# Kernel optimization log

Hardware: AMD Instinct MI355X
Metric: run time of the kernel (lower is better)

The kernel has to match this reference:

```python
import jax, jax.numpy as jnp
import numpy as np

B = 4096          # agents
T = 16            # input_length
GH, GW = 13, 13   # grid_size
ENC = 64          # encoder_size
INP = 32          # input_embedding
DYN = 32          # dynamic_embedding
SOC = 64          # soc_embedding_size
DEC = 128         # decoder_size
K = 32            # occupied grid cells (neighbors) per agent
NNB = B * K       # total neighbors


def lrelu(x):
    return jnp.where(x >= 0, x, 0.1 * x)


def lstm_scan(x, Wih, Whh, bih, bhh, return_seq=False):
    # PyTorch LSTM gate order: i, f, g, o. x: [T, N, in]
    N = x.shape[1]
    H = Whh.shape[1]
    xg = jnp.einsum('tni,gi->tng', x, Wih) + bih + bhh  # precompute input part

    def step(carry, g_in):
        h, c = carry
        g = g_in + h @ Whh.T
        i, f, gg, o = jnp.split(g, 4, axis=-1)
        c = jax.nn.sigmoid(f) * c + jax.nn.sigmoid(i) * jnp.tanh(gg)
        h = jax.nn.sigmoid(o) * jnp.tanh(c)
        return (h, c), (h if return_seq else None)

    h0 = jnp.zeros((N, H), x.dtype)
    (h, _), hs = jax.lax.scan(step, (h0, h0), xg)
    return hs if return_seq else h


def setup_inputs() -> dict:
    key = jax.random.key(0)
    ks = jax.random.split(key, 16)

    def lin(k, o, i):
        k1, k2 = jax.random.split(k)
        s = 1.0 / np.sqrt(i)
        return (jax.random.uniform(k1, (o, i), minval=-s, maxval=s),
                jax.random.uniform(k2, (o,), minval=-s, maxval=s))

    W_inp, b_inp = lin(ks[0], INP, 2)
    W_dym, b_dym = lin(ks[1], DYN, ENC)
    W_sp, b_sp = lin(ks[2], SOC, GH * GW * ENC)
    W_out, b_out = lin(ks[3], 5, DEC)
    Wih, bih = lin(ks[4], 4 * ENC, INP)
    Whh, bhh = lin(ks[5], 4 * ENC, ENC)
    dWih, dbih = lin(ks[6], 4 * DEC, SOC + DYN)
    dWhh, dbhh = lin(ks[7], 4 * DEC, DEC)

    hist_batch = jax.random.normal(ks[8], (T, B, 2), dtype=jnp.float32)
    nbrs_batch = jax.random.normal(ks[9], (T, NNB, 2), dtype=jnp.float32)

    # mask: exactly K occupied grid cells per agent; each occupied cell is True
    # across all ENC channels so masked_scatter_ places exactly one neighbor
    # hidden vector per occupied cell (True count == NNB * ENC).
    rng = np.random.default_rng(0)
    idx = np.argsort(rng.random((B, GH * GW)), axis=1)[:, :K]
    cells = np.zeros((B, GH * GW), dtype=bool)
    np.put_along_axis(cells, idx, True, axis=1)
    mask_batch = jnp.asarray(
        np.broadcast_to(cells.reshape(B, GH, GW, 1), (B, GH, GW, ENC)))

    return dict(hist_batch=hist_batch, nbrs_batch=nbrs_batch,
                W_inp=W_inp, b_inp=b_inp, Wih=Wih, Whh=Whh, bih=bih, bhh=bhh,
                W_dym=W_dym, b_dym=b_dym, W_sp=W_sp, b_sp=b_sp,
                dWih=dWih, dWhh=dWhh, dbih=dbih, dbhh=dbhh,
                W_out=W_out, b_out=b_out, mask_batch=mask_batch)


def reference(hist_batch, nbrs_batch, W_inp, b_inp, Wih, Whh, bih, bhh,
              W_dym, b_dym, W_sp, b_sp, dWih, dWhh, dbih, dbhh,
              W_out, b_out, mask_batch):
    # history encoder
    hist_h = lstm_scan(lrelu(hist_batch @ W_inp.T + b_inp), Wih, Whh, bih, bhh)  # [B,ENC]
    hist_enc = lrelu(hist_h @ W_dym.T + b_dym)                                   # [B,DYN]

    # neighbor encoder (shared LSTM)
    nbrs_h = lstm_scan(lrelu(nbrs_batch @ W_inp.T + b_inp), Wih, Whh, bih, bhh)  # [NNB,ENC]

    # masked_scatter_: fill True positions (row-major order) with nbrs_h values
    mflat = mask_batch.reshape(-1)
    src = nbrs_h.reshape(-1)
    pos = jnp.cumsum(mflat) - 1
    soc = jnp.where(mflat, src[jnp.clip(pos, 0, src.shape[0] - 1)],
                    jnp.zeros((), src.dtype))
    soc = soc.reshape(mask_batch.shape)                 # [B,GH,GW,ENC]
    soc = soc.transpose(0, 3, 2, 1)                     # permute(0,3,2,1)
    soc = soc.reshape(soc.shape[0], -1)                 # [B, ENC*GW*GH]
    social = lrelu(soc @ W_sp.T + b_sp)                 # [B,SOC]

    enc = jnp.concatenate([hist_enc, social], axis=1)   # [B, DYN+SOC]
    enc_seq = jnp.broadcast_to(enc, (T,) + enc.shape)   # repeat(T,1,1)
    dec = lstm_scan(enc_seq, dWih, dWhh, dbih, dbhh, return_seq=True)  # [T,B,DEC]
    out = dec.transpose(1, 0, 2) @ W_out.T + b_out      # [B,T,5]

    # outputActivation: mu_x, mu_y, exp(sig_x), exp(sig_y), tanh(rho)
    muX, muY, sX, sY, rho = jnp.split(out, 5, axis=2)
    return jnp.concatenate(
        [muX, muY, jnp.exp(sX), jnp.exp(sY), jnp.tanh(rho)], axis=2)
```

## Files before the change

kernel.cpp:

```cpp
#include <hip/hip_runtime.h>
#include <hip/hip_bf16.h>

typedef _Float16 half8 __attribute__((ext_vector_type(8)));
typedef _Float16 half2v __attribute__((ext_vector_type(2)));
typedef float f32x4 __attribute__((ext_vector_type(4)));

constexpr float L2E   = 1.44269504088896340736f;
constexpr float SC_LO = 4096.0f;
constexpr float IV_LO = 1.0f / 4096.0f;

#define MFMA16(a,b,c) __builtin_amdgcn_mfma_f32_16x16x32_f16((a),(b),(c),0,0,0)

__device__ __forceinline__ float fexp2(float x){ float r; asm("v_exp_f32 %0, %1":"=v"(r):"v"(x)); return r; }
__device__ __forceinline__ float frcp(float x){ float r; asm("v_rcp_f32 %0, %1":"=v"(r):"v"(x)); return r; }

__device__ __forceinline__ float sigm_s(float y){ return frcp(1.0f + fexp2(-y)); }
__device__ __forceinline__ float tanh_s(float y){ return 1.0f - 2.0f*frcp(fexp2(y) + 1.0f); }

__global__ __launch_bounds__(256, 2)
void mega_enc_kernel(const float* __restrict__ xh,
                     const float* __restrict__ xn,
                     const float* __restrict__ W_inp,
                     const float* __restrict__ b_inp,
                     const float* __restrict__ Wih,
                     const float* __restrict__ Whh,
                     const float* __restrict__ bih,
                     const float* __restrict__ bhh,
                     const float* __restrict__ W_sp,
                     const void*  __restrict__ mask_raw,
                     float* __restrict__ outh,
                     float* __restrict__ outn,
                     _Float16* __restrict__ WspT,
                     unsigned char* __restrict__ pos)
{
    __shared__ _Float16 h_hi[2][64*72];
    __shared__ _Float16 h_ls[2][64*72];
    const int tid = threadIdx.x;
    const int bid = blockIdx.x;

    if (bid >= 2112) {
        if (bid < 2112 + 2704) {
            const int idx = (bid - 2112) * 256 + tid;
            if (idx < 64 * 10816) {
                const int s = idx / 10816, cidx = idx % 10816;
                const int e = cidx / 169, p = cidx % 169;
                WspT[((size_t)p*64 + e)*64 + s] = (_Float16)W_sp[idx];
            }
        } else {
            const int agent = (bid - 4816) * 4 + (tid >> 6);
            const int l = tid & 63;
            if (agent < 4096) {
                if (l < 32) pos[agent*32 + l] = 0;
                const unsigned char* raw = (const unsigned char*)mask_raw;
                const int* mi = (const int*)mask_raw;
                int mism = 0;
#pragma unroll
                for (int ch = 0; ch < 3; ++ch) {
                    const int cc = ch*64 + l;
                    if (cc < 169) {
                        const unsigned char b0 = raw[cc*64], b1 = raw[cc*64 + 1];
                        mism |= (b0 != 0 && b1 == 0) ? 1 : 0;
                    }
                }
                const bool is_i32 = (__ballot(mism != 0) != 0ull);
                int base = 0;
#pragma unroll
                for (int ch = 0; ch < 3; ++ch) {
                    const int cc = ch*64 + l;
                    bool occ = false;
                    if (cc < 169) {
                        const size_t ei = (size_t)agent * 10816 + (size_t)cc * 64;
                        occ = is_i32 ? (mi[ei] != 0) : (raw[ei] != 0);
                    }
                    const unsigned long long bal = __ballot(occ);
                    if (occ) {
                        const int rank = base + __popcll(bal & ((1ull << l) - 1ull));
                        const int gh = cc / 13, gw = cc % 13;
                        if (rank < 32)
                            pos[agent*32 + rank] = (unsigned char)(gw*13 + gh);
                    }
                    base += __popcll(bal);
                }
            }
        }
        return;
    }

    const int w   = tid >> 6;
    const int l   = tid & 63;
    const int l15 = l & 15, lhi = l >> 4;

    const bool is_hist = (bid < 64);
    const float* x = is_hist ? xh : xn;
    float* out     = is_hist ? outh : outn;
    const int N    = is_hist ? 4096 : 131072;
    const int rbase = (is_hist ? bid : (bid - 64)) * 64;

    half8 whhH[4][2], whhLs[4][2];
    half8 wihH[4];
    float bias[4];
#pragma unroll
    for (int g = 0; g < 4; ++g) {
        const int col = 16*(w + 4*g) + l15;
        const float sc = (g == 2) ? 2.0f*L2E : L2E;
#pragma unroll
        for (int kh = 0; kh < 2; ++kh)
#pragma unroll
            for (int j = 0; j < 8; ++j) {
                const float v = Whh[col*64 + kh*32 + lhi*8 + j] * sc;
                const _Float16 hi = (_Float16)v;
                whhH[g][kh][j]  = hi;
                whhLs[g][kh][j] = (_Float16)((v - (float)hi) * SC_LO);
            }
#pragma unroll
        for (int j = 0; j < 8; ++j)
            wihH[g][j] = (_Float16)(Wih[col*32 + lhi*8 + j] * sc);
        bias[g] = (bih[col] + bhh[col]) * sc;
    }
    half2v w01[8];
    float bb[8];
#pragma unroll
    for (int j = 0; j < 8; ++j) {
        const int k = lhi*8 + j;
        w01[j][0] = (_Float16)W_inp[k*2 + 0];
        w01[j][1] = (_Float16)W_inp[k*2 + 1];
        bb[j] = b_inp[k];
    }

    float c[4][4];
#pragma unroll
    for (int m = 0; m < 4; ++m)
#pragma unroll
        for (int j = 0; j < 4; ++j) c[m][j] = 0.0f;

    const float2* xp = (const float2*)x;
    float2 xc[4];
#pragma unroll
    for (int m = 0; m < 4; ++m)
        xc[m] = xp[(size_t)0*N + rbase + 16*m + l15];

#pragma unroll 1
    for (int t = 0; t < 16; ++t) {
        const int rdb = (t + 1) & 1;
        const int wrb = t & 1;
#pragma unroll
        for (int m = 0; m < 4; ++m) {
            half8 eh;
#pragma unroll
            for (int j = 0; j < 8; ++j) {
                float v = xc[m].x * (float)w01[j][0] + xc[m].y * (float)w01[j][1] + bb[j];
                v = fmaxf(v, 0.1f * v);
                eh[j] = (_Float16)v;
            }
            f32x4 a0[4], a2[4];
#pragma unroll
            for (int g = 0; g < 4; ++g) {
                a0[g] = (f32x4){bias[g], bias[g], bias[g], bias[g]};
                a2[g] = (f32x4){0.f, 0.f, 0.f, 0.f};
            }
#pragma unroll
            for (int g = 0; g < 4; ++g)
                a0[g] = MFMA16(eh, wihH[g], a0[g]);
            if (t > 0) {
#pragma unroll
                for (int kh = 0; kh < 2; ++kh) {
                    const int off = (16*m + l15)*72 + kh*32 + lhi*8;
                    half8 ah = *(const half8*)&h_hi[rdb][off];
                    half8 as = *(const half8*)&h_ls[rdb][off];
#pragma unroll
                    for (int g = 0; g < 4; ++g) {
                        a0[g] = MFMA16(ah, whhH[g][kh],  a0[g]);
                        a2[g] = MFMA16(ah, whhLs[g][kh], a2[g]);
                        a2[g] = MFMA16(as, whhH[g][kh],  a2[g]);
                    }
                }
            }
#pragma unroll
            for (int j = 0; j < 4; ++j) {
                const float pi = a0[0][j] + a2[0][j]*IV_LO;
                const float pf = a0[1][j] + a2[1][j]*IV_LO;
                const float pg = a0[2][j] + a2[2][j]*IV_LO;
                const float po = a0[3][j] + a2[3][j]*IV_LO;
                const float si = sigm_s(pi);
                const float sf = sigm_s(pf);
                const float tg = tanh_s(pg);
                const float so = sigm_s(po);
                const float cc = sf * c[m][j] + si * tg;
                c[m][j] = cc;
                const float hv = so * tanh_s(2.0f*L2E*cc);
                const int idx = (16*m + lhi*4 + j)*72 + 16*w + l15;
                const _Float16 hi = (_Float16)hv;
                h_hi[wrb][idx] = hi;
                h_ls[wrb][idx] = (_Float16)((hv - (float)hi) * SC_LO);
            }
        }
        __syncthreads();
        if (t < 15) {
#pragma unroll
            for (int m = 0; m < 4; ++m)
                xc[m] = xp[(size_t)(t+1)*N + rbase + 16*m + l15];
        }
    }
    {
        const int row = tid >> 2, c0 = (tid & 3) * 16;
        const size_t g = (size_t)(rbase + row) * 64 + c0;
#pragma unroll
        for (int i = 0; i < 16; ++i) {
            const int idx = row*72 + c0 + i;
            out[g + i] = (float)h_hi[1][idx] + (float)h_ls[1][idx] * IV_LO;
        }
    }
}

__global__ __launch_bounds__(256)
void social_kernel(const float* __restrict__ nh,
                   const float* __restrict__ hh,
                   const _Float16* __restrict__ WspT,
                   const float* __restrict__ b_sp,
                   const float* __restrict__ W_dym,
                   const float* __restrict__ b_dym,
                   const unsigned char* __restrict__ pos,
                   float* __restrict__ enc)
{
    __shared__ float part[4][64];
    __shared__ unsigned char pl[32];
    const int tid = threadIdx.x, b = blockIdx.x;
    if (tid < 32) {
        const int p = pos[b*32 + tid];
        pl[tid] = (unsigned char)(p > 168 ? 0 : p);
    }
    __syncthreads();
    const int s = tid & 63, kq = tid >> 6;
    float a = 0.f;
    for (int kk = 0; kk < 8; ++kk) {
        const int k = kq*8 + kk;
        const float* nr = nh + ((size_t)b*32 + k) * 64;
        const _Float16* wp = WspT + (size_t)pl[k] * 4096 + s;
#pragma unroll
        for (int e = 0; e < 64; ++e) a += nr[e] * (float)wp[(size_t)e * 64];
    }
    part[kq][s] = a;
    __syncthreads();
    if (tid < 64) {
        const float v = part[0][tid] + part[1][tid] + part[2][tid] + part[3][tid] + b_sp[tid];
        enc[(size_t)b * 96 + 32 + tid] = fmaxf(v, 0.1f * v);
    } else if (tid >= 64 && tid < 96) {
        const int so = tid - 64;
        float ah = b_dym[so];
        const float* hr = hh + (size_t)b * 64;
        const float* wr = W_dym + (size_t)so * 64;
#pragma unroll
        for (int e = 0; e < 64; ++e) ah += hr[e] * wr[e];
        enc[(size_t)b * 96 + so] = fmaxf(ah, 0.1f * ah);
    }
}

__global__ __launch_bounds__(512, 1)
void decoder_kernel(const float* __restrict__ enc,
                    const float* __restrict__ dWih,
                    const float* __restrict__ dWhh,
                    const float* __restrict__ dbih,
                    const float* __restrict__ dbhh,
                    const float* __restrict__ W_out,
                    const float* __restrict__ b_out,
                    float* __restrict__ outp)
{
    __shared__ float enc_lds[16*100];
    __shared__ _Float16 hh_t[16*136];
    __shared__ _Float16 hl_t[16*136];
    __shared__ float wout[5*132];
    __shared__ float bout[5];
    __shared__ float part[16][5][4];
    const int tid = threadIdx.x;
    const int w = tid >> 6, l = tid & 63, l15 = l & 15, lhi = l >> 4;
    const int rb = blockIdx.x * 16;

    if (tid < 384) {
        const int row = tid / 24, ch = tid % 24;
        *(float4*)&enc_lds[row*100 + ch*4] = *(const float4*)&enc[(size_t)(rb + row)*96 + ch*4];
    }
    for (int i = tid; i < 640; i += 512) { const int j = i / 128, e = i % 128; wout[j*132 + e] = W_out[i]; }
    if (tid < 5) bout[tid] = b_out[tid];
    __syncthreads();

    half8 whhH[4][4], whhLs[4][4];
    f32x4 xg0[4], xg2[4];
#pragma unroll
    for (int g = 0; g < 4; ++g) {
        const int col = 16*(8*g + w) + l15;
        const float sc = (g == 2) ? 2.0f*L2E : L2E;
#pragma unroll
        for (int kh = 0; kh < 4; ++kh)
#pragma unroll
            for (int j = 0; j < 8; ++j) {
                const float v = dWhh[col*128 + kh*32 + lhi*8 + j] * sc;
                const _Float16 hi = (_Float16)v;
                whhH[g][kh][j]  = hi;
                whhLs[g][kh][j] = (_Float16)((v - (float)hi) * SC_LO);
            }
        const float bv = (dbih[col] + dbhh[col]) * sc;
        xg0[g] = (f32x4){bv, bv, bv, bv};
        xg2[g] = (f32x4){0.f, 0.f, 0.f, 0.f};
    }
#pragma unroll
    for (int kh = 0; kh < 3; ++kh) {
        half8 eh, els;
#pragma unroll
        for (int j = 0; j < 8; ++j) {
            const float v = enc_lds[l15*100 + kh*32 + lhi*8 + j];
            const _Float16 hi = (_Float16)v;
            eh[j]  = hi;
            els[j] = (_Float16)((v - (float)hi) * SC_LO);
        }
#pragma unroll
        for (int g = 0; g < 4; ++g) {
            const int col = 16*(8*g + w) + l15;
            const float sc = (g == 2) ? 2.0f*L2E : L2E;
            half8 bH, bLs;
#pragma unroll
            for (int j = 0; j < 8; ++j) {
                const float v = dWih[col*96 + kh*32 + lhi*8 + j] * sc;
                const _Float16 hi = (_Float16)v;
                bH[j]  = hi;
                bLs[j] = (_Float16)((v - (float)hi) * SC_LO);
            }
            xg0[g] = MFMA16(eh,  bH,  xg0[g]);
            xg2[g] = MFMA16(eh,  bLs, xg2[g]);
            xg2[g] = MFMA16(els, bH,  xg2[g]);
        }
    }
    f32x4 xg[4];
#pragma unroll
    for (int g = 0; g < 4; ++g)
#pragma unroll
        for (int j = 0; j < 4; ++j) xg[g][j] = xg0[g][j] + xg2[g][j]*IV_LO;

    float c[4] = {0.f, 0.f, 0.f, 0.f};
#pragma unroll 1
    for (int t = 0; t < 16; ++t) {
        f32x4 a0[4], a2[4];
#pragma unroll
        for (int g = 0; g < 4; ++g) { a0[g] = xg[g]; a2[g] = (f32x4){0.f,0.f,0.f,0.f}; }
        if (t > 0) {
#pragma unroll
            for (int kh = 0; kh < 4; ++kh) {
                const int off = l15*136 + kh*32 + lhi*8;
                half8 ah = *(const half8*)&hh_t[off];
                half8 as = *(const half8*)&hl_t[off];
#pragma unroll
                for (int g = 0; g < 4; ++g) {
                    a0[g] = MFMA16(ah, whhH[g][kh],  a0[g]);
                    a2[g] = MFMA16(ah, whhLs[g][kh], a2[g]);
                    a2[g] = MFMA16(as, whhH[g][kh],  a2[g]);
                }
            }
        }
        float hnew[4];
#pragma unroll
        for (int j = 0; j < 4; ++j) {
            const float pi = a0[0][j] + a2[0][j]*IV_LO;
            const float pf = a0[1][j] + a2[1][j]*IV_LO;
            const float pg = a0[2][j] + a2[2][j]*IV_LO;
            const float po = a0[3][j] + a2[3][j]*IV_LO;
            const float si = sigm_s(pi);
            const float sf = sigm_s(pf);
            const float tg = tanh_s(pg);
            const float so = sigm_s(po);
            const float cc = sf * c[j] + si * tg;
            c[j] = cc;
            hnew[j] = so * tanh_s(2.0f*L2E*cc);
        }
        __syncthreads();
#pragma unroll
        for (int j = 0; j < 4; ++j) {
            const int idx = (lhi*4 + j)*136 + 16*w + l15;
            const float v = hnew[j];
            const _Float16 hi = (_Float16)v;
            hh_t[idx] = hi;
            hl_t[idx] = (_Float16)((v - (float)hi) * SC_LO);
        }
        __syncthreads();
        if (tid < 320) {
            const int row = tid / 20, rem = tid % 20, j5 = rem / 4, q = rem % 4;
            float pacc = 0.0f;
#pragma unroll
            for (int e = 0; e < 32; ++e) {
                const int idx = row*136 + q*32 + e;
                pacc += ((float)hh_t[idx] + (float)hl_t[idx]*IV_LO) * wout[j5*132 + q*32 + e];
            }
            part[row][j5][q] = pacc;
        }
        __syncthreads();
        if (tid < 80) {
            const int row = tid / 5, j5 = tid % 5;
            float v = part[row][j5][0] + part[row][j5][1] + part[row][j5][2] + part[row][j5][3] + bout[j5];
            if (j5 == 2 || j5 == 3) v = fexp2(v * L2E);
            else if (j5 == 4)       v = tanh_s(2.0f*L2E*v);
            outp[((size_t)(rb + row)*16 + t)*5 + j5] = v;
        }
    }
}

extern "C" void kernel_launch(void* const* d_in, const int* in_sizes, int n_in,
                              void* d_out, int out_size, void* d_ws, size_t ws_size,
                              hipStream_t stream) {
    const float* hist  = (const float*)d_in[0];
    const float* nbrs  = (const float*)d_in[1];
    const float* W_inp = (const float*)d_in[2];
    const float* b_inp = (const float*)d_in[3];
    const float* Wih   = (const float*)d_in[4];
    const float* Whh   = (const float*)d_in[5];
    const float* bih   = (const float*)d_in[6];
    const float* bhh   = (const float*)d_in[7];
    const float* W_dym = (const float*)d_in[8];
    const float* b_dym = (const float*)d_in[9];
    const float* W_sp  = (const float*)d_in[10];
    const float* b_sp  = (const float*)d_in[11];
    const float* dWih  = (const float*)d_in[12];
    const float* dWhh  = (const float*)d_in[13];
    const float* dbih  = (const float*)d_in[14];
    const float* dbhh  = (const float*)d_in[15];
    const float* W_out = (const float*)d_in[16];
    const float* b_out = (const float*)d_in[17];
    const void* mask   = (const void*)d_in[18];

    char* ws = (char*)d_ws;
    float* nh32        = (float*)(ws);
    float* hh32        = (float*)(ws + 33554432);
    _Float16* WspT16   = (_Float16*)(ws + 34603008);
    unsigned char* pos = (unsigned char*)(ws + 35987456);
    float* enc32       = (float*)(ws + 36118528);

    mega_enc_kernel<<<5840, 256, 0, stream>>>(hist, nbrs, W_inp, b_inp, Wih, Whh, bih, bhh,
                                              W_sp, mask, hh32, nh32, WspT16, pos);
    social_kernel<<<4096, 256, 0, stream>>>(nh32, hh32, WspT16, b_sp, W_dym, b_dym, pos, enc32);
    decoder_kernel<<<256, 512, 0, stream>>>(enc32, dWih, dWhh, dbih, dbhh, W_out, b_out,
                                            (float*)d_out);
}
```

Measured before the change: 482.3 us.

## Store encoder hidden states as fp16 and use fdot2 in social projection

The encoder kernels now write their final hidden states as fp16, keeping only the high half of the split-precision pair instead of reconstructing fp32. This halves the intermediate buffer traffic between the encoder and social kernels. The transposed social weight is re-laid out so each thread reads a contiguous 64-element row, and the inner product uses packed half2 dot instructions. Dropping the low-order correction lowers the precision of the hidden states passed downstream.

```diff
diff --git a/kernel.cpp b/kernel.cpp
--- a/kernel.cpp
+++ b/kernel.cpp
@@ -16,6 +16,14 @@
 
 __device__ __forceinline__ float sigm_s(float y){ return frcp(1.0f + fexp2(-y)); }
 __device__ __forceinline__ float tanh_s(float y){ return 1.0f - 2.0f*frcp(fexp2(y) + 1.0f); }
+
+__device__ __forceinline__ float dot2acc(half2v a, half2v b, float c) {
+#if __has_builtin(__builtin_amdgcn_fdot2)
+    return __builtin_amdgcn_fdot2(a, b, c, false);
+#else
+    return c + (float)a[0]*(float)b[0] + (float)a[1]*(float)b[1];
+#endif
+}
 
 __global__ __launch_bounds__(256, 2)
 void mega_enc_kernel(const float* __restrict__ xh,
@@ -28,8 +36,8 @@
                      const float* __restrict__ bhh,
                      const float* __restrict__ W_sp,
                      const void*  __restrict__ mask_raw,
-                     float* __restrict__ outh,
-                     float* __restrict__ outn,
+                     _Float16* __restrict__ outh,
+                     _Float16* __restrict__ outn,
                      _Float16* __restrict__ WspT,
                      unsigned char* __restrict__ pos)
 {
@@ -44,7 +52,7 @@
             if (idx < 64 * 10816) {
                 const int s = idx / 10816, cidx = idx % 10816;
                 const int e = cidx / 169, p = cidx % 169;
-                WspT[((size_t)p*64 + e)*64 + s] = (_Float16)W_sp[idx];
+                WspT[((size_t)p*64 + s)*64 + e] = (_Float16)W_sp[idx];
             }
         } else {
             const int agent = (bid - 4816) * 4 + (tid >> 6);
@@ -91,10 +99,10 @@
     const int l15 = l & 15, lhi = l >> 4;
 
     const bool is_hist = (bid < 64);
-    const float* x = is_hist ? xh : xn;
-    float* out     = is_hist ? outh : outn;
-    const int N    = is_hist ? 4096 : 131072;
-    const int rbase = (is_hist ? bid : (bid - 64)) * 64;
+    const float* x    = is_hist ? xh : xn;
+    _Float16* out     = is_hist ? outh : outn;
+    const int N       = is_hist ? 4096 : 131072;
+    const int rbase   = (is_hist ? bid : (bid - 64)) * 64;
 
     half8 whhH[4][2], whhLs[4][2];
     half8 wihH[4];
@@ -204,17 +212,16 @@
     {
         const int row = tid >> 2, c0 = (tid & 3) * 16;
         const size_t g = (size_t)(rbase + row) * 64 + c0;
-#pragma unroll
-        for (int i = 0; i < 16; ++i) {
-            const int idx = row*72 + c0 + i;
-            out[g + i] = (float)h_hi[1][idx] + (float)h_ls[1][idx] * IV_LO;
-        }
+        half8 v0 = *(const half8*)&h_hi[1][row*72 + c0];
+        half8 v1 = *(const half8*)&h_hi[1][row*72 + c0 + 8];
+        *(half8*)&out[g]     = v0;
+        *(half8*)&out[g + 8] = v1;
     }
 }
 
 __global__ __launch_bounds__(256)
-void social_kernel(const float* __restrict__ nh,
-                   const float* __restrict__ hh,
+void social_kernel(const _Float16* __restrict__ nh,
+                   const _Float16* __restrict__ hh,
                    const _Float16* __restrict__ WspT,
                    const float* __restrict__ b_sp,
                    const float* __restrict__ W_dym,
@@ -234,10 +241,11 @@
     float a = 0.f;
     for (int kk = 0; kk < 8; ++kk) {
         const int k = kq*8 + kk;
-        const float* nr = nh + ((size_t)b*32 + k) * 64;
-        const _Float16* wp = WspT + (size_t)pl[k] * 4096 + s;
-#pragma unroll
-        for (int e = 0; e < 64; ++e) a += nr[e] * (float)wp[(size_t)e * 64];
+        const half2v* nr = (const half2v*)(nh + ((size_t)b*32 + k) * 64);
+        const half2v* wp = (const half2v*)(WspT + ((size_t)pl[k]*64 + s) * 64);
+#pragma unroll
+        for (int e2 = 0; e2 < 32; ++e2)
+            a = dot2acc(nr[e2], wp[e2], a);
     }
     part[kq][s] = a;
     __syncthreads();
@@ -247,10 +255,10 @@
     } else if (tid >= 64 && tid < 96) {
         const int so = tid - 64;
         float ah = b_dym[so];
-        const float* hr = hh + (size_t)b * 64;
+        const _Float16* hr = hh + (size_t)b * 64;
         const float* wr = W_dym + (size_t)so * 64;
 #pragma unroll
-        for (int e = 0; e < 64; ++e) ah += hr[e] * wr[e];
+        for (int e = 0; e < 64; ++e) ah += (float)hr[e] * wr[e];
         enc[(size_t)b * 96 + so] = fmaxf(ah, 0.1f * ah);
     }
 }
@@ -425,15 +433,15 @@
     const void* mask   = (const void*)d_in[18];
 
     char* ws = (char*)d_ws;
-    float* nh32        = (float*)(ws);
-    float* hh32        = (float*)(ws + 33554432);
-    _Float16* WspT16   = (_Float16*)(ws + 34603008);
-    unsigned char* pos = (unsigned char*)(ws + 35987456);
-    float* enc32       = (float*)(ws + 36118528);
+    _Float16* nh16     = (_Float16*)(ws);
+    _Float16* hh16     = (_Float16*)(ws + 16777216);
+    _Float16* WspT16   = (_Float16*)(ws + 17301504);
+    unsigned char* pos = (unsigned char*)(ws + 18685952);
+    float* enc32       = (float*)(ws + 18817024);
 
     mega_enc_kernel<<<5840, 256, 0, stream>>>(hist, nbrs, W_inp, b_inp, Wih, Whh, bih, bhh,
-                                              W_sp, mask, hh32, nh32, WspT16, pos);
-    social_kernel<<<4096, 256, 0, stream>>>(nh32, hh32, WspT16, b_sp, W_dym, b_dym, pos, enc32);
+                                              W_sp, mask, hh16, nh16, WspT16, pos);
+    social_kernel<<<4096, 256, 0, stream>>>(nh16, hh16, WspT16, b_sp, W_dym, b_dym, pos, enc32);
     decoder_kernel<<<256, 512, 0, stream>>>(enc32, dWih, dWhh, dbih, dbhh, W_out, b_out,
                                             (float*)d_out);
 }
```

Measured after the change: 531.2 us. +10.1%, slower.
